# Kernel optimization log

Measured on AMD Instinct MI355X. Metric: run time of the kernel, lower is better.

The kernel has to match this reference:

```python
import jax, jax.numpy as jnp
import numpy as np
import math

B, T, D = 4, 2048, 1024
H, DK, DV = 4, 128, 256
KD, VD = H * DK, H * DV
LOG_T_REF = math.log(512.0)
EPS = 1e-5


def setup_inputs() -> dict:
    key = jax.random.key(0)
    ks = jax.random.split(key, 8)
    hs = jax.random.normal(ks[0], (B, T, D), dtype=jnp.float32)
    Wq = jax.random.normal(ks[1], (KD, D), dtype=jnp.float32) / math.sqrt(D)
    Wk = jax.random.normal(ks[2], (KD, D), dtype=jnp.float32) / math.sqrt(D)
    Wv = jax.random.normal(ks[3], (VD, D), dtype=jnp.float32) / math.sqrt(D)
    Wg = jax.random.normal(ks[4], (VD, D), dtype=jnp.float32) / math.sqrt(D)
    Wa = jax.random.normal(ks[5], (KD, D), dtype=jnp.float32) / math.sqrt(D)
    Wo = jax.random.normal(ks[6], (D, VD), dtype=jnp.float32) / math.sqrt(VD)
    # _post_init: A_log_base = 0, A_log_delta = log(exp(gap)-1+1e-6), gap = log(16)/(H-1)
    gap = math.log(16.0) / (H - 1)
    A_log_base = jnp.zeros((), dtype=jnp.float32)
    A_log_delta = jnp.full((H - 1,), math.log(math.exp(gap) - 1.0 + 1e-6), dtype=jnp.float32)
    # dt_bias init (inverse-softplus of dt sampled loguniform in [1e-3, 1e-1])
    rng = np.random.default_rng(0)
    dt = np.exp(rng.random(KD) * (math.log(0.1) - math.log(0.001)) + math.log(0.001))
    dt = np.clip(dt, 1e-4, None)
    dt_bias = jnp.asarray(dt + np.log(-np.expm1(-dt)), dtype=jnp.float32)
    g_norm_weight = jnp.ones((VD,), dtype=jnp.float32)
    return {"hidden_states": hs, "Wq": Wq, "Wk": Wk, "Wv": Wv, "Wg": Wg, "Wa": Wa,
            "Wo": Wo, "A_log_base": A_log_base, "A_log_delta": A_log_delta,
            "dt_bias": dt_bias, "g_norm_weight": g_norm_weight}


def _gla_forward(hidden_states, Wq, Wk, Wv, Wg, Wa, Wo, A_log_base, A_log_delta, dt_bias, g_norm_weight):
    b, t, _ = hidden_states.shape
    q = (hidden_states @ Wq.T).reshape(b, t, H, DK)
    k = (hidden_states @ Wk.T).reshape(b, t, H, DK)
    v = (hidden_states @ Wv.T).reshape(b, t, H, DV)
    a = (hidden_states @ Wa.T).reshape(b, t, H, DK)

    # geometric spectral allocation: A_log[h] = base + cumsum(softplus(delta))
    A_log = A_log_base + jnp.concatenate([jnp.zeros((1,), dtype=A_log_delta.dtype),
                                          jnp.cumsum(jax.nn.softplus(A_log_delta))])
    # per-head log-decay gate: gk = -exp(A_log) * softplus(a + dt_bias)  [b,t,h,dk]
    gk = -jnp.exp(A_log)[None, None, :, None] * jax.nn.softplus(a + dt_bias.reshape(H, DK)[None, None])

    # analytical position-adaptive alpha
    cum = A_log - A_log[0]
    kk = jnp.arange(H, dtype=A_log.dtype)
    mean_gap = cum[-1] / (H - 1)
    taper = (H - 1 - kk) / (H - 1)
    alpha = jnp.clip(taper + (cum - kk * mean_gap) / LOG_T_REF, 0.0, 1.0)  # [H]
    pos = jnp.arange(1, t + 1, dtype=jnp.float32)
    gk = gk * (pos[:, None] ** (-alpha[None, :]))[None, :, :, None]

    # gated linear attention recurrence: S_t = exp(gk_t)*S_{t-1} + k_t^T v_t ; o_t = q_t S_t
    scale = DK ** -0.5
    qT = jnp.moveaxis(q, 1, 0) * scale  # [t,b,h,dk]
    kT = jnp.moveaxis(k, 1, 0)
    vT = jnp.moveaxis(v, 1, 0)
    gT = jnp.moveaxis(gk, 1, 0)

    def step(S, inp):
        qt, kt, vt, gt = inp
        S = S * jnp.exp(gt)[..., None] + kt[..., None] * vt[..., None, :]  # [b,h,dk,dv]
        ot = jnp.einsum('bhk,bhkv->bhv', qt, S)
        return S, ot

    S0 = jnp.zeros((b, H, DK, DV), dtype=jnp.float32)
    _, oT = jax.lax.scan(step, S0, (qT, kT, vT, gT))
    o = jnp.moveaxis(oT, 0, 1)  # [b,t,h,dv]

    # fused RMSNorm + swish output gate (per head over dv)
    g = (hidden_states @ Wg.T).reshape(b, t, H, DV)
    o = o * jax.lax.rsqrt(jnp.mean(o * o, axis=-1, keepdims=True) + EPS)
    o = o * g_norm_weight.reshape(H, DV)[None, None] * (g * jax.nn.sigmoid(g))
    return o.reshape(b, t, VD) @ Wo.T


def reference(hidden_states, Wq, Wk, Wv, Wg, Wa, Wo, A_log_base, A_log_delta, dt_bias, g_norm_weight):
    return _gla_forward(hidden_states, Wq, Wk, Wv, Wg, Wa, Wo, A_log_base, A_log_delta, dt_bias, g_norm_weight)
```

## Files before the change

### kernel.cpp

```cpp
#include <hip/hip_runtime.h>
#include <math.h>

#define Bn   4
#define Tn   2048
#define Dn   1024
#define Hn   4
#define DKn  128
#define DVn  256
#define KDn  512
#define VDn  1024
#define NROWS 8192
#define NCC  32
#define CLEN 64
#define LOG_T_REF_F 6.2383246250395075f

using bf16x8 = __attribute__((ext_vector_type(8))) short;
using f32x4  = __attribute__((ext_vector_type(4))) float;

__device__ __forceinline__ float softplus_f(float x) {
    return fmaxf(x, 0.0f) + log1pf(expf(-fabsf(x)));
}
__device__ __forceinline__ ushort f2bf(float f) {
    unsigned u = __float_as_uint(f);
    u = (u + 0x7fffu + ((u >> 16) & 1u)) >> 16;
    return (ushort)u;
}
__device__ __forceinline__ float bf2f(ushort u) {
    return __uint_as_float((unsigned)u << 16);
}
__device__ __forceinline__ void gload16(const void* g, void* l) {
    __builtin_amdgcn_global_load_lds(
        (const __attribute__((address_space(1))) unsigned*)g,
        (__attribute__((address_space(3))) unsigned*)l, 16, 0, 0);
}

struct CastArgs {
    const float* src[7];
    ushort* dst[7];
    int cum[8];
};
__global__ __launch_bounds__(256) void cast_all(CastArgs a) {
    const int total = a.cum[7];
    for (int i = blockIdx.x * 256 + threadIdx.x; i < total; i += gridDim.x * 256) {
        int s = 0;
        #pragma unroll
        for (int k = 1; k < 7; ++k) s += (i >= a.cum[k]) ? 1 : 0;
        const int off = i - a.cum[s];
        float4 v = *(const float4*)&a.src[s][(size_t)off * 4];
        ushort4 u;
        u.x = f2bf(v.x); u.y = f2bf(v.y); u.z = f2bf(v.z); u.w = f2bf(v.w);
        *(ushort4*)&a.dst[s][(size_t)off * 4] = u;
    }
}

template<int MODE, int NX>
__global__ __launch_bounds__(256) void mm3(const ushort* __restrict__ A,
    const ushort* __restrict__ Bw, float* __restrict__ C,
    float* __restrict__ Cv, ushort* __restrict__ C2, float* __restrict__ Eo,
    const float* __restrict__ dt_bias, const float* __restrict__ A_log_base,
    const float* __restrict__ A_log_delta)
{
    __shared__ __align__(16) ushort As[8][128][8];
    __shared__ __align__(16) ushort Bs[8][128][8];
    const int raw = blockIdx.x;
    const int nwg = NX * 64;
    const int l = (raw & 7) * (nwg >> 3) + (raw >> 3);
    const int bx = l % NX, by = l / NX;
    const int tid = threadIdx.x;
    const int lane = tid & 63, w = tid >> 6;
    const int l15 = lane & 15, lg = lane >> 4;
    const int wr = (w >> 1) << 6, wc = (w & 1) << 6;
    const int row0 = by << 7, col0 = bx << 7;

    const ushort* A0 = A  + (size_t)(row0 + lane) * Dn + w * 8;
    const ushort* A1 = A  + (size_t)(row0 + 64 + lane) * Dn + w * 8;
    const ushort* B0 = Bw + (size_t)(col0 + lane) * Dn + w * 8;
    const ushort* B1 = Bw + (size_t)(col0 + 64 + lane) * Dn + w * 8;

    f32x4 acc[4][4];
    #pragma unroll
    for (int m = 0; m < 4; ++m)
        #pragma unroll
        for (int n = 0; n < 4; ++n)
            acc[m][n] = (f32x4){0.f, 0.f, 0.f, 0.f};

    for (int kt = 0; kt < Dn; kt += 64) {
        __syncthreads();
        gload16(A0 + kt,      &As[w][0][0]);
        gload16(A0 + kt + 32, &As[w + 4][0][0]);
        gload16(A1 + kt,      &As[w][64][0]);
        gload16(A1 + kt + 32, &As[w + 4][64][0]);
        gload16(B0 + kt,      &Bs[w][0][0]);
        gload16(B0 + kt + 32, &Bs[w + 4][0][0]);
        gload16(B1 + kt,      &Bs[w][64][0]);
        gload16(B1 + kt + 32, &Bs[w + 4][64][0]);
        __syncthreads();
        #pragma unroll
        for (int ks = 0; ks < 2; ++ks) {
            bf16x8 af[4], bv[4];
            #pragma unroll
            for (int m = 0; m < 4; ++m)
                af[m] = *(const bf16x8*)&As[ks * 4 + lg][wr + m * 16 + l15][0];
            #pragma unroll
            for (int n = 0; n < 4; ++n)
                bv[n] = *(const bf16x8*)&Bs[ks * 4 + lg][wc + n * 16 + l15][0];
            #pragma unroll
            for (int m = 0; m < 4; ++m)
                #pragma unroll
                for (int n = 0; n < 4; ++n)
                    acc[m][n] = __builtin_amdgcn_mfma_f32_16x16x32_bf16(af[m], bv[n], acc[m][n], 0, 0, 0);
        }
    }

    if (MODE == 1 && col0 >= 1024 && col0 < 1536) {
        const float base_ = A_log_base[0];
        const float s0 = softplus_f(A_log_delta[0]);
        const float s1 = softplus_f(A_log_delta[1]);
        const float s2 = softplus_f(A_log_delta[2]);
        const float c3 = s0 + s1 + s2;
        const float mg = c3 * (1.0f / 3.0f);
        float pf[4][4];
        #pragma unroll
        for (int m = 0; m < 4; ++m) {
            const int row = row0 + wr + m * 16 + lg * 4;
            #pragma unroll
            for (int r = 0; r < 4; ++r) {
                const int t = (row + r) & (Tn - 1);
                pf[m][r] = logf((float)(t + 1));
            }
        }
        #pragma unroll
        for (int n = 0; n < 4; ++n) {
            const int dk = col0 - 1024 + wc + n * 16 + l15;
            const int h = dk >> 7;
            const float cumh = (h == 0) ? 0.f : (h == 1) ? s0 : (h == 2) ? s0 + s1 : c3;
            float alpha = (float)(3 - h) * (1.0f / 3.0f)
                        + (cumh - (float)h * mg) * (1.0f / LOG_T_REF_F);
            alpha = fminf(fmaxf(alpha, 0.0f), 1.0f);
            const float expA = expf(base_ + cumh);
            const float db = dt_bias[dk];
            #pragma unroll
            for (int m = 0; m < 4; ++m) {
                const int row = row0 + wr + m * 16 + lg * 4;
                #pragma unroll
                for (int r = 0; r < 4; ++r) {
                    const float p = expf(-alpha * pf[m][r]);
                    Eo[(size_t)(row + r) * KDn + dk] =
                        -expA * softplus_f(acc[m][n][r] + db) * p;
                }
            }
        }
    } else if (MODE == 1 && col0 >= 1536) {
        const int cv0 = col0 - 1536;
        if (cv0 < 1024) {
            #pragma unroll
            for (int m = 0; m < 4; ++m) {
                const int row = row0 + wr + m * 16 + lg * 4;
                #pragma unroll
                for (int n = 0; n < 4; ++n) {
                    const int col = cv0 + wc + n * 16 + l15;
                    #pragma unroll
                    for (int r = 0; r < 4; ++r)
                        Cv[(size_t)(row + r) * 1024 + col] = acc[m][n][r];
                }
            }
        } else {
            #pragma unroll
            for (int m = 0; m < 4; ++m) {
                const int row = row0 + wr + m * 16 + lg * 4;
                #pragma unroll
                for (int n = 0; n < 4; ++n) {
                    const int col = cv0 - 1024 + wc + n * 16 + l15;
                    #pragma unroll
                    for (int r = 0; r < 4; ++r)
                        C2[(size_t)(row + r) * 1024 + col] = f2bf(acc[m][n][r]);
                }
            }
        }
    } else {
        const float s = (MODE == 1 && col0 < 512) ? 0.08838834764831845f : 1.0f;
        #pragma unroll
        for (int m = 0; m < 4; ++m) {
            const int row = row0 + wr + m * 16 + lg * 4;
            #pragma unroll
            for (int n = 0; n < 4; ++n) {
                const int col = col0 + wc + n * 16 + l15;
                #pragma unroll
                for (int r = 0; r < 4; ++r)
                    C[(size_t)(row + r) * 1024 + col] = acc[m][n][r] * s;
            }
        }
    }
}

__global__ __launch_bounds__(1024) void gla_chunk(
    float* qk, const float* __restrict__ Gb, const float* __restrict__ vb,
    float* __restrict__ o, float* __restrict__ Sl, float* __restrict__ Dc)
{
    extern __shared__ __align__(16) char smem[];
    float*  g    = (float*)smem;
    ushort* qraw = (ushort*)(smem + 33792);
    ushort* kraw = (ushort*)(smem + 51200);
    ushort* Qb   = (ushort*)(smem + 68608);
    ushort* Koff = (ushort*)(smem + 86016);
    ushort* KhT  = (ushort*)(smem + 112128);
    ushort* At   = (ushort*)(smem + 130560);
    ushort* VT   = (ushort*)smem;
    float*  qsum = (float*)(smem + 86016);

    const int bid = blockIdx.x;
    const int co = bid >> 4, bh = bid & 15;
    const int b = bh >> 2, h = bh & 3;
    const int tid = threadIdx.x;
    const int w = tid >> 6, lane = tid & 63;
    const int l15 = lane & 15, lg = lane >> 4;
    const size_t rowbase = (size_t)(b * Tn + co * CLEN);

    float c16[16];
    int dk1 = 0, qr1 = 0;
    if (tid < 512) {
        dk1 = tid & 127; qr1 = tid >> 7;
        const float* gp = Gb + (rowbase + qr1 * 16) * 512 + h * 128 + dk1;
        float run = 0.f;
        #pragma unroll
        for (int s = 0; s < 16; ++s) { run += gp[(size_t)s * 512]; c16[s] = run; }
        qsum[qr1 * 128 + dk1] = run;
    }
    __syncthreads();
    if (tid < 512) {
        float pre = 0.f;
        for (int r = 0; r < qr1; ++r) pre += qsum[r * 128 + dk1];
        #pragma unroll
        for (int s = 0; s < 16; ++s) g[(qr1 * 16 + s) * 132 + dk1] = c16[s] + pre;
    }
    __syncthreads();

    #pragma unroll
    for (int it = 0; it < 8; ++it) {
        const int idx = tid + it * 1024;
        const int t = idx >> 7, dk = idx & 127;
        const float gi = g[t * 132 + dk];
        const size_t qaddr = (rowbase + t) * 1024 + h * 128 + dk;
        const float qv = qk[qaddr];
        const float gr = (t < 16) ? 0.f : g[(16 * (t >> 4) - 1) * 132 + dk];
        Qb[t * 136 + dk] = f2bf(qv * __expf(gi - gr));
        qraw[t * 136 + dk] = f2bf(qv);
        qk[qaddr] = qv * __expf(gi);
        const float kv = qk[qaddr + 512];
        kraw[t * 136 + dk] = f2bf(kv);
        KhT[dk * 72 + t] = f2bf(kv * __expf(g[63 * 132 + dk] - gi));
        if (t < 16) Koff[t * 136 + dk]        = f2bf(kv * __expf(g[15 * 132 + dk] - gi));
        if (t < 32) Koff[(16 + t) * 136 + dk] = f2bf(kv * __expf(g[31 * 132 + dk] - gi));
        if (t < 48) Koff[(48 + t) * 136 + dk] = f2bf(kv * __expf(g[47 * 132 + dk] - gi));
    }
    for (int i = tid; i < 2304; i += 1024) ((int*)At)[i] = 0;
    if (tid < 128)
        Dc[(co * 16 + bh) * 128 + tid] = __expf(g[63 * 132 + tid]);
    __syncthreads();

    if (w < 6) {
        const int Tt[6] = {16, 32, 32, 48, 48, 48};
        const int Ss[6] = { 0,  0, 16,  0, 16, 32};
        const int Kb[6] = { 0, 16, 16, 48, 48, 48};
        const int T = Tt[w], S = Ss[w], KB = Kb[w];
        f32x4 acc = (f32x4){0.f, 0.f, 0.f, 0.f};
        #pragma unroll
        for (int kk = 0; kk < 4; ++kk) {
            bf16x8 a  = *(const bf16x8*)&Qb[(T + l15) * 136 + kk * 32 + lg * 8];
            bf16x8 bb = *(const bf16x8*)&Koff[(KB + S + l15) * 136 + kk * 32 + lg * 8];
            acc = __builtin_amdgcn_mfma_f32_16x16x32_bf16(a, bb, acc, 0, 0, 0);
        }
        #pragma unroll
        for (int r = 0; r < 4; ++r)
            At[(T + lg * 4 + r) * 72 + S + l15] = f2bf(acc[r]);
    } else if (w < 14) {
        const int d = (w - 6) >> 1, hf = (w - 6) & 1;
        #pragma unroll
        for (int pp = 0; pp < 2; ++pp) {
            const int p = hf * 128 + pp * 64 + lane;
            const int i_ = p >> 4, j_ = p & 15;
            if (j_ <= i_) {
                const int ti = d * 16 + i_, tj = d * 16 + j_;
                float a = 0.f;
                for (int dk = 0; dk < 128; ++dk) {
                    const float qf = bf2f(qraw[ti * 136 + dk]);
                    const float kf = bf2f(kraw[tj * 136 + dk]);
                    a += qf * kf * __expf(g[ti * 132 + dk] - g[tj * 132 + dk]);
                }
                At[ti * 72 + tj] = f2bf(a);
            }
        }
    }
    __syncthreads();

    {
        const int dv4 = (tid & 63) * 4, tseg = tid >> 6;
        float4 vv[4];
        #pragma unroll
        for (int s = 0; s < 4; ++s)
            vv[s] = *(const float4*)&vb[(rowbase + tseg * 4 + s) * 1024 + h * 256 + dv4];
        const float* vf = (const float*)vv;
        #pragma unroll
        for (int c = 0; c < 4; ++c) {
            int lo = (unsigned)f2bf(vf[0 * 4 + c]) | ((unsigned)f2bf(vf[1 * 4 + c]) << 16);
            int hi = (unsigned)f2bf(vf[2 * 4 + c]) | ((unsigned)f2bf(vf[3 * 4 + c]) << 16);
            *(int2*)((char*)VT + (size_t)(dv4 + c) * 144 + tseg * 8) = make_int2(lo, hi);
        }
    }
    __syncthreads();

    float* sp = Sl + (((size_t)co * 16 + bh) << 15);
    for (int id = w; id < 192; id += 16) {
        if (id < 64) {
            const int mt = id >> 4, nt = id & 15;
            f32x4 acc = (f32x4){0.f, 0.f, 0.f, 0.f};
            #pragma unroll
            for (int kk = 0; kk < 2; ++kk) {
                bf16x8 a  = *(const bf16x8*)&At[(mt * 16 + l15) * 72 + kk * 32 + lg * 8];
                bf16x8 bb = *(const bf16x8*)&VT[(nt * 16 + l15) * 72 + kk * 32 + lg * 8];
                acc = __builtin_amdgcn_mfma_f32_16x16x32_bf16(a, bb, acc, 0, 0, 0);
            }
            #pragma unroll
            for (int r = 0; r < 4; ++r)
                o[(rowbase + mt * 16 + lg * 4 + r) * 1024 + h * 256 + nt * 16 + l15] = acc[r];
        } else {
            const int sid = id - 64;
            const int mt = sid >> 4, nt = sid & 15;
            f32x4 acc = (f32x4){0.f, 0.f, 0.f, 0.f};
            #pragma unroll
            for (int kk = 0; kk < 2; ++kk) {
                bf16x8 a  = *(const bf16x8*)&KhT[(mt * 16 + l15) * 72 + kk * 32 + lg * 8];
                bf16x8 bb = *(const bf16x8*)&VT[(nt * 16 + l15) * 72 + kk * 32 + lg * 8];
                acc = __builtin_amdgcn_mfma_f32_16x16x32_bf16(a, bb, acc, 0, 0, 0);
            }
            #pragma unroll
            for (int r = 0; r < 4; ++r)
                sp[(size_t)(mt * 16 + lg * 4 + r) * 256 + nt * 16 + l15] = acc[r];
        }
    }
}

__global__ __launch_bounds__(256) void combine(float* __restrict__ Sl,
                                               const float* __restrict__ Dc) {
    const int bh = blockIdx.y;
    const int e4 = blockIdx.x * 256 + threadIdx.x;
    const int dk = e4 >> 6;
    float4 s = make_float4(0.f, 0.f, 0.f, 0.f);
    #pragma unroll 4
    for (int c = 0; c < NCC; ++c) {
        float4* p = (float4*)(Sl + (((size_t)c * 16 + bh) << 15)) + e4;
        float4 local = *p;
        const float d = Dc[(c * 16 + bh) * DKn + dk];
        *p = s;
        s.x = s.x * d + local.x;  s.y = s.y * d + local.y;
        s.z = s.z * d + local.z;  s.w = s.w * d + local.w;
    }
}

__global__ __launch_bounds__(256, 4) void fixup(const float* __restrict__ qt,
    const float* __restrict__ Sl, float* __restrict__ o)
{
    __shared__ __align__(16) float Aq[16][68];
    __shared__ __align__(16) float Bs[16][68];
    const int raw = blockIdx.x;
    const int l = (raw & 7) * 256 + (raw >> 3);
    const int dvt = l & 3, bh = (l >> 2) & 15, co = l >> 6;
    const int b = bh >> 2, h = bh & 3;
    const int tid = threadIdx.x;
    const int tx = tid & 15, ty = tid >> 4;
    const int t0 = co * CLEN;
    const int dv0 = dvt * 64;

    const float* qbase = qt + (size_t)(b * Tn + t0) * 1024 + h * 128;
    const float* sbase = Sl + (((size_t)co * 16 + bh) << 15) + dv0;

    float acc[4][4] = {};
    for (int k0 = 0; k0 < DKn; k0 += 16) {
        __syncthreads();
        {
            const int t = tid >> 2, kk4 = (tid & 3) << 2;
            float4 a = *(const float4*)&qbase[(size_t)t * 1024 + k0 + kk4];
            Aq[kk4 + 0][t] = a.x; Aq[kk4 + 1][t] = a.y;
            Aq[kk4 + 2][t] = a.z; Aq[kk4 + 3][t] = a.w;
        }
        {
            const int dk = tid >> 4, dvq = (tid & 15) << 2;
            *(float4*)&Bs[dk][dvq] = *(const float4*)&sbase[(size_t)(k0 + dk) * 256 + dvq];
        }
        __syncthreads();
        #pragma unroll
        for (int kk = 0; kk < 16; ++kk) {
            float4 a  = *(const float4*)&Aq[kk][ty * 4];
            float4 bv = *(const float4*)&Bs[kk][tx * 4];
            float ar[4] = {a.x, a.y, a.z, a.w};
            float br[4] = {bv.x, bv.y, bv.z, bv.w};
            #pragma unroll
            for (int i = 0; i < 4; ++i)
                #pragma unroll
                for (int j = 0; j < 4; ++j)
                    acc[i][j] += ar[i] * br[j];
        }
    }
    float* obp = o + (size_t)(b * Tn + t0) * 1024 + h * 256 + dv0;
    #pragma unroll
    for (int i = 0; i < 4; ++i) {
        float* row = obp + (size_t)(ty * 4 + i) * 1024 + tx * 4;
        float4 c = *(float4*)row;
        c.x += acc[i][0]; c.y += acc[i][1];
        c.z += acc[i][2]; c.w += acc[i][3];
        *(float4*)row = c;
    }
}

__global__ __launch_bounds__(256) void rms_gate(const float* __restrict__ o,
    const ushort* __restrict__ gbf, const float* __restrict__ wt,
    ushort* __restrict__ obf)
{
    const int tid = threadIdx.x;
    const int w = tid >> 6, lane = tid & 63;
    const int row = blockIdx.x * 4 + w;
    const int n = row >> 2, h = row & 3;
    const size_t ob_base = (size_t)n * VDn + h * DVn + lane * 4;

    float4 o4 = *(const float4*)&o[ob_base];
    float ss = o4.x*o4.x + o4.y*o4.y + o4.z*o4.z + o4.w*o4.w;
    #pragma unroll
    for (int m = 1; m < 64; m <<= 1) ss += __shfl_xor(ss, m);
    const float r = rsqrtf(ss * (1.0f / DVn) + 1e-5f);

    ushort4 gu = *(const ushort4*)&gbf[ob_base];
    float gx = bf2f(gu.x), gy = bf2f(gu.y), gz = bf2f(gu.z), gw = bf2f(gu.w);
    float4 w4 = *(const float4*)&wt[h * DVn + lane * 4];
    ushort4 u;
    u.x = f2bf(o4.x * r * w4.x * (gx / (1.0f + expf(-gx))));
    u.y = f2bf(o4.y * r * w4.y * (gy / (1.0f + expf(-gy))));
    u.z = f2bf(o4.z * r * w4.z * (gz / (1.0f + expf(-gz))));
    u.w = f2bf(o4.w * r * w4.w * (gw / (1.0f + expf(-gw))));
    *(ushort4*)&obf[ob_base] = u;
}

extern "C" void kernel_launch(void* const* d_in, const int* in_sizes, int n_in,
                              void* d_out, int out_size, void* d_ws, size_t ws_size,
                              hipStream_t stream) {
    const float* hs          = (const float*)d_in[0];
    const float* Wq          = (const float*)d_in[1];
    const float* Wk          = (const float*)d_in[2];
    const float* Wv          = (const float*)d_in[3];
    const float* Wg          = (const float*)d_in[4];
    const float* Wa          = (const float*)d_in[5];
    const float* Wo          = (const float*)d_in[6];
    const float* A_log_base  = (const float*)d_in[7];
    const float* A_log_delta = (const float*)d_in[8];
    const float* dt_bias     = (const float*)d_in[9];
    const float* gnw         = (const float*)d_in[10];
    float* out = (float*)d_out;

    char* ws = (char*)d_ws;
    float*  qk   = (float*)(ws);
    float*  vb   = (float*)(ws + ((size_t)32  << 20));
    float*  Gbuf = (float*)(ws + ((size_t)64  << 20));
    float*  Sl   = (float*)(ws + ((size_t)80  << 20));
    float*  ob   = (float*)(ws + ((size_t)144 << 20));
    ushort* hsb  = (ushort*)(ws + ((size_t)144 << 20));
    ushort* gbf  = (ushort*)(ws + ((size_t)176 << 20));
    ushort* Wcat = (ushort*)(ws + ((size_t)192 << 20));
    ushort* Wob  = (ushort*)(ws + ((size_t)199 << 20));
    float*  Dc   = (float*)(ws + ((size_t)201 << 20));
    ushort* obf  = (ushort*)qk;

    CastArgs ca;
    ca.src[0] = hs; ca.src[1] = Wq; ca.src[2] = Wk; ca.src[3] = Wa;
    ca.src[4] = Wv; ca.src[5] = Wg; ca.src[6] = Wo;
    ca.dst[0] = hsb;
    ca.dst[1] = Wcat;
    ca.dst[2] = Wcat + (size_t)512 * 1024;
    ca.dst[3] = Wcat + (size_t)1024 * 1024;
    ca.dst[4] = Wcat + (size_t)1536 * 1024;
    ca.dst[5] = Wcat + (size_t)2560 * 1024;
    ca.dst[6] = Wob;
    const int n4s[7] = {NROWS * Dn / 4, KDn * Dn / 4, KDn * Dn / 4, KDn * Dn / 4,
                        VDn * Dn / 4, VDn * Dn / 4, VDn * Dn / 4};
    ca.cum[0] = 0;
    for (int i = 0; i < 7; ++i) ca.cum[i + 1] = ca.cum[i] + n4s[i];
    cast_all<<<2048, 256, 0, stream>>>(ca);

    mm3<1,28><<<1792, 256, 0, stream>>>(hsb, Wcat, qk, vb, gbf, Gbuf,
                                        dt_bias, A_log_base, A_log_delta);

    (void)hipFuncSetAttribute((const void*)gla_chunk,
                              hipFuncAttributeMaxDynamicSharedMemorySize, 139776);
    gla_chunk<<<512, 1024, 139776, stream>>>(qk, Gbuf, vb, ob, Sl, Dc);
    combine<<<dim3(32, 16), 256, 0, stream>>>(Sl, Dc);
    fixup<<<2048, 256, 0, stream>>>(qk, Sl, ob);

    rms_gate<<<NROWS * Hn / 4, 256, 0, stream>>>(ob, gbf, gnw, obf);
    mm3<0,8><<<512, 256, 0, stream>>>(obf, Wob, out, nullptr, nullptr, nullptr,
                                      nullptr, nullptr, nullptr);
}
```

Baseline: 309.1 us.

## Use 256x256 tiles with double-buffered LDS pipeline for fused projection GEMM

Replaces the 128x128-tile projection GEMM with a 512-thread kernel that computes 256x256 tiles, takes a K step of 64, and double-buffers the LDS loads. The next stage is prefetched while the current one is consumed, synchronised with explicit vmcnt waits and barriers. Larger tiles raise arithmetic intensity and cut global reloads. The prefetch is meant to hide load latency. In exchange, each block uses 130KB of LDS and a large accumulator array, so occupancy drops, and the grid shrinks to 448 blocks, which may leave CUs unevenly loaded. The output GEMM becomes a specialised copy of the old kernel with no functional change.

```diff
diff --git a/kernel.cpp b/kernel.cpp
--- a/kernel.cpp
+++ b/kernel.cpp
@@ -53,19 +53,161 @@
     }
 }
 
-template<int MODE, int NX>
-__global__ __launch_bounds__(256) void mm3(const ushort* __restrict__ A,
+template<int NX>
+__global__ __launch_bounds__(512) void mm_big(const ushort* __restrict__ A,
     const ushort* __restrict__ Bw, float* __restrict__ C,
     float* __restrict__ Cv, ushort* __restrict__ C2, float* __restrict__ Eo,
     const float* __restrict__ dt_bias, const float* __restrict__ A_log_base,
     const float* __restrict__ A_log_delta)
 {
+    extern __shared__ __align__(16) char smem2[];
+    ushort* sm = (ushort*)smem2;
+    const int raw = blockIdx.x;
+    const int nwg = NX * 32;
+    const int l = (raw & 7) * (nwg >> 3) + (raw >> 3);
+    const int bx = l % NX, by = l / NX;
+    const int tid = threadIdx.x;
+    const int w = tid >> 6, lane = tid & 63;
+    const int l15 = lane & 15, lg = lane >> 4;
+    const int wr = w >> 2, wc = w & 3;
+    const int row0 = by << 8, col0 = bx << 8;
+
+    const ushort* Asrc = A  + (size_t)(row0 + lane) * Dn + w * 8;
+    const ushort* Bsrc = Bw + (size_t)(col0 + lane) * Dn + w * 8;
+
+    f32x4 acc[8][4];
+    #pragma unroll
+    for (int m = 0; m < 8; ++m)
+        #pragma unroll
+        for (int n = 0; n < 4; ++n)
+            acc[m][n] = (f32x4){0.f, 0.f, 0.f, 0.f};
+
+    #define STAGE(buf, kt)                                                        \
+    {                                                                             \
+        ushort* ab_ = sm + (buf) * 33280 + w * 2080;                              \
+        ushort* bb_ = ab_ + 16640;                                                \
+        _Pragma("unroll")                                                         \
+        for (int g_ = 0; g_ < 4; ++g_) {                                          \
+            gload16(Asrc + (size_t)g_ * 64 * Dn + (kt), ab_ + g_ * 512);          \
+            gload16(Bsrc + (size_t)g_ * 64 * Dn + (kt), bb_ + g_ * 512);          \
+        }                                                                         \
+    }
+
+    STAGE(0, 0)
+    for (int it = 0; it < 16; ++it) {
+        const int cur = it & 1;
+        if (it < 15) {
+            STAGE(cur ^ 1, (it + 1) * 64)
+            asm volatile("s_waitcnt vmcnt(8)" ::: "memory");
+        } else {
+            asm volatile("s_waitcnt vmcnt(0)" ::: "memory");
+        }
+        asm volatile("s_barrier" ::: "memory");
+        const ushort* ab = sm + cur * 33280;
+        const ushort* bb = ab + 16640;
+        #pragma unroll
+        for (int ks = 0; ks < 2; ++ks) {
+            bf16x8 af[8], bv[4];
+            #pragma unroll
+            for (int m = 0; m < 8; ++m)
+                af[m] = *(const bf16x8*)(ab + (ks * 4 + lg) * 2080
+                                            + (wr * 128 + m * 16 + l15) * 8);
+            #pragma unroll
+            for (int n = 0; n < 4; ++n)
+                bv[n] = *(const bf16x8*)(bb + (ks * 4 + lg) * 2080
+                                            + (wc * 64 + n * 16 + l15) * 8);
+            #pragma unroll
+            for (int m = 0; m < 8; ++m)
+                #pragma unroll
+                for (int n = 0; n < 4; ++n)
+                    acc[m][n] = __builtin_amdgcn_mfma_f32_16x16x32_bf16(af[m], bv[n], acc[m][n], 0, 0, 0);
+        }
+        asm volatile("s_barrier" ::: "memory");
+    }
+    #undef STAGE
+
+    if (col0 >= 1024 && col0 < 1536) {
+        const float base_ = A_log_base[0];
+        const float s0 = softplus_f(A_log_delta[0]);
+        const float s1 = softplus_f(A_log_delta[1]);
+        const float s2 = softplus_f(A_log_delta[2]);
+        const float c3 = s0 + s1 + s2;
+        const float mg = c3 * (1.0f / 3.0f);
+        #pragma unroll
+        for (int m = 0; m < 8; ++m) {
+            const int row = row0 + wr * 128 + m * 16 + lg * 4;
+            float pf[4];
+            #pragma unroll
+            for (int r = 0; r < 4; ++r) {
+                const int t = (row + r) & (Tn - 1);
+                pf[r] = logf((float)(t + 1));
+            }
+            #pragma unroll
+            for (int n = 0; n < 4; ++n) {
+                const int dk = col0 - 1024 + wc * 64 + n * 16 + l15;
+                const int h = dk >> 7;
+                const float cumh = (h == 0) ? 0.f : (h == 1) ? s0 : (h == 2) ? s0 + s1 : c3;
+                float alpha = (float)(3 - h) * (1.0f / 3.0f)
+                            + (cumh - (float)h * mg) * (1.0f / LOG_T_REF_F);
+                alpha = fminf(fmaxf(alpha, 0.0f), 1.0f);
+                const float expA = expf(base_ + cumh);
+                const float db = dt_bias[dk];
+                #pragma unroll
+                for (int r = 0; r < 4; ++r) {
+                    const float p = expf(-alpha * pf[r]);
+                    Eo[(size_t)(row + r) * KDn + dk] =
+                        -expA * softplus_f(acc[m][n][r] + db) * p;
+                }
+            }
+        }
+    } else if (col0 >= 2560) {
+        #pragma unroll
+        for (int m = 0; m < 8; ++m) {
+            const int row = row0 + wr * 128 + m * 16 + lg * 4;
+            #pragma unroll
+            for (int n = 0; n < 4; ++n) {
+                const int col = col0 - 2560 + wc * 64 + n * 16 + l15;
+                #pragma unroll
+                for (int r = 0; r < 4; ++r)
+                    C2[(size_t)(row + r) * 1024 + col] = f2bf(acc[m][n][r]);
+            }
+        }
+    } else if (col0 >= 1536) {
+        #pragma unroll
+        for (int m = 0; m < 8; ++m) {
+            const int row = row0 + wr * 128 + m * 16 + lg * 4;
+            #pragma unroll
+            for (int n = 0; n < 4; ++n) {
+                const int col = col0 - 1536 + wc * 64 + n * 16 + l15;
+                #pragma unroll
+                for (int r = 0; r < 4; ++r)
+                    Cv[(size_t)(row + r) * 1024 + col] = acc[m][n][r];
+            }
+        }
+    } else {
+        const float s = (col0 < 512) ? 0.08838834764831845f : 1.0f;
+        #pragma unroll
+        for (int m = 0; m < 8; ++m) {
+            const int row = row0 + wr * 128 + m * 16 + lg * 4;
+            #pragma unroll
+            for (int n = 0; n < 4; ++n) {
+                const int col = col0 + wc * 64 + n * 16 + l15;
+                #pragma unroll
+                for (int r = 0; r < 4; ++r)
+                    C[(size_t)(row + r) * 1024 + col] = acc[m][n][r] * s;
+            }
+        }
+    }
+}
+
+__global__ __launch_bounds__(256) void mm_out(const ushort* __restrict__ A,
+    const ushort* __restrict__ Bw, float* __restrict__ C)
+{
     __shared__ __align__(16) ushort As[8][128][8];
     __shared__ __align__(16) ushort Bs[8][128][8];
     const int raw = blockIdx.x;
-    const int nwg = NX * 64;
-    const int l = (raw & 7) * (nwg >> 3) + (raw >> 3);
-    const int bx = l % NX, by = l / NX;
+    const int l = (raw & 7) * 64 + (raw >> 3);
+    const int bx = l % 8, by = l / 8;
     const int tid = threadIdx.x;
     const int lane = tid & 63, w = tid >> 6;
     const int l15 = lane & 15, lg = lane >> 4;
@@ -111,84 +253,15 @@
                     acc[m][n] = __builtin_amdgcn_mfma_f32_16x16x32_bf16(af[m], bv[n], acc[m][n], 0, 0, 0);
         }
     }
-
-    if (MODE == 1 && col0 >= 1024 && col0 < 1536) {
-        const float base_ = A_log_base[0];
-        const float s0 = softplus_f(A_log_delta[0]);
-        const float s1 = softplus_f(A_log_delta[1]);
-        const float s2 = softplus_f(A_log_delta[2]);
-        const float c3 = s0 + s1 + s2;
-        const float mg = c3 * (1.0f / 3.0f);
-        float pf[4][4];
-        #pragma unroll
-        for (int m = 0; m < 4; ++m) {
-            const int row = row0 + wr + m * 16 + lg * 4;
-            #pragma unroll
-            for (int r = 0; r < 4; ++r) {
-                const int t = (row + r) & (Tn - 1);
-                pf[m][r] = logf((float)(t + 1));
-            }
-        }
+    #pragma unroll
+    for (int m = 0; m < 4; ++m) {
+        const int row = row0 + wr + m * 16 + lg * 4;
         #pragma unroll
         for (int n = 0; n < 4; ++n) {
-            const int dk = col0 - 1024 + wc + n * 16 + l15;
-            const int h = dk >> 7;
-            const float cumh = (h == 0) ? 0.f : (h == 1) ? s0 : (h == 2) ? s0 + s1 : c3;
-            float alpha = (float)(3 - h) * (1.0f / 3.0f)
-                        + (cumh - (float)h * mg) * (1.0f / LOG_T_REF_F);
-            alpha = fminf(fmaxf(alpha, 0.0f), 1.0f);
-            const float expA = expf(base_ + cumh);
-            const float db = dt_bias[dk];
-            #pragma unroll
-            for (int m = 0; m < 4; ++m) {
-                const int row = row0 + wr + m * 16 + lg * 4;
-                #pragma unroll
-                for (int r = 0; r < 4; ++r) {
-                    const float p = expf(-alpha * pf[m][r]);
-                    Eo[(size_t)(row + r) * KDn + dk] =
-                        -expA * softplus_f(acc[m][n][r] + db) * p;
-                }
-            }
-        }
-    } else if (MODE == 1 && col0 >= 1536) {
-        const int cv0 = col0 - 1536;
-        if (cv0 < 1024) {
-            #pragma unroll
-            for (int m = 0; m < 4; ++m) {
-                const int row = row0 + wr + m * 16 + lg * 4;
-                #pragma unroll
-                for (int n = 0; n < 4; ++n) {
-                    const int col = cv0 + wc + n * 16 + l15;
-                    #pragma unroll
-                    for (int r = 0; r < 4; ++r)
-                        Cv[(size_t)(row + r) * 1024 + col] = acc[m][n][r];
-                }
-            }
-        } else {
-            #pragma unroll
-            for (int m = 0; m < 4; ++m) {
-                const int row = row0 + wr + m * 16 + lg * 4;
-                #pragma unroll
-                for (int n = 0; n < 4; ++n) {
-                    const int col = cv0 - 1024 + wc + n * 16 + l15;
-                    #pragma unroll
-                    for (int r = 0; r < 4; ++r)
-                        C2[(size_t)(row + r) * 1024 + col] = f2bf(acc[m][n][r]);
-                }
-            }
-        }
-    } else {
-        const float s = (MODE == 1 && col0 < 512) ? 0.08838834764831845f : 1.0f;
-        #pragma unroll
-        for (int m = 0; m < 4; ++m) {
-            const int row = row0 + wr + m * 16 + lg * 4;
-            #pragma unroll
-            for (int n = 0; n < 4; ++n) {
-                const int col = col0 + wc + n * 16 + l15;
-                #pragma unroll
-                for (int r = 0; r < 4; ++r)
-                    C[(size_t)(row + r) * 1024 + col] = acc[m][n][r] * s;
-            }
+            const int col = col0 + wc + n * 16 + l15;
+            #pragma unroll
+            for (int r = 0; r < 4; ++r)
+                C[(size_t)(row + r) * 1024 + col] = acc[m][n][r];
         }
     }
 }
@@ -484,8 +557,10 @@
     for (int i = 0; i < 7; ++i) ca.cum[i + 1] = ca.cum[i] + n4s[i];
     cast_all<<<2048, 256, 0, stream>>>(ca);
 
-    mm3<1,28><<<1792, 256, 0, stream>>>(hsb, Wcat, qk, vb, gbf, Gbuf,
-                                        dt_bias, A_log_base, A_log_delta);
+    (void)hipFuncSetAttribute((const void*)mm_big<14>,
+                              hipFuncAttributeMaxDynamicSharedMemorySize, 133120);
+    mm_big<14><<<448, 512, 133120, stream>>>(hsb, Wcat, qk, vb, gbf, Gbuf,
+                                             dt_bias, A_log_base, A_log_delta);
 
     (void)hipFuncSetAttribute((const void*)gla_chunk,
                               hipFuncAttributeMaxDynamicSharedMemorySize, 139776);
@@ -494,6 +569,5 @@
     fixup<<<2048, 256, 0, stream>>>(qk, Sl, ob);
 
     rms_gate<<<NROWS * Hn / 4, 256, 0, stream>>>(ob, gbf, gnw, obf);
-    mm3<0,8><<<512, 256, 0, stream>>>(obf, Wob, out, nullptr, nullptr, nullptr,
-                                      nullptr, nullptr, nullptr);
-}
+    mm_out<<<512, 256, 0, stream>>>(obf, Wob, out);
+}
```

Result: no change. 313.0 us (+1.3%).
